# Kernel tuning notes

Hardware: AMD Instinct MI355X
Metric: run time of the kernel (lower is better)

## Reference

```python
import jax, jax.numpy as jnp
import numpy as np

N = 100000   # nodes
E = 1600000  # edges (avg degree 16)
F_IN = 128
HID = 128
C_OUT = 10
BN_EPS = 1e-5


def setup_inputs() -> dict:
    key = jax.random.key(0)
    ks = jax.random.split(key, 20)
    x = jax.random.normal(ks[0], (N, F_IN), jnp.float32)
    src = jax.random.randint(ks[1], (E,), 0, N)
    dst = jax.random.randint(ks[2], (E,), 0, N)
    def lin(k, fi, fo):
        return jax.random.normal(k, (fi, fo), jnp.float32) * (1.0 / np.sqrt(fi))
    inp = {
        "x": x, "src": src, "dst": dst,
        "W1": lin(ks[3], F_IN, HID), "b1": jnp.zeros((HID,), jnp.float32),
        "g1": jax.random.normal(ks[4], (HID,), jnp.float32) * 0.1 + 1.0,
        "be1": jax.random.normal(ks[5], (HID,), jnp.float32) * 0.1,
        "m1": jax.random.normal(ks[6], (HID,), jnp.float32) * 0.1,
        "v1": jax.random.uniform(ks[7], (HID,), jnp.float32, 0.5, 1.5),
        "W2": lin(ks[8], HID, HID), "b2": jnp.zeros((HID,), jnp.float32),
        "g2": jax.random.normal(ks[9], (HID,), jnp.float32) * 0.1 + 1.0,
        "be2": jax.random.normal(ks[10], (HID,), jnp.float32) * 0.1,
        "m2": jax.random.normal(ks[11], (HID,), jnp.float32) * 0.1,
        "v2": jax.random.uniform(ks[12], (HID,), jnp.float32, 0.5, 1.5),
        "W3": lin(ks[13], HID, C_OUT), "b3": jnp.zeros((C_OUT,), jnp.float32),
    }
    return inp


def _gcn_conv(x, W, b, src, dst):
    # PyG GCNConv: linear, add self-loops, symmetric deg^-1/2 normalization, scatter-add.
    h = x @ W                                            # [N, out]
    deg = jax.ops.segment_sum(jnp.ones((E,), h.dtype), dst, num_segments=N) + 1.0  # self-loop
    dinv = jax.lax.rsqrt(deg)                            # deg^{-1/2}, [N]
    coef = dinv[src] * dinv[dst]                         # per-edge norm, [E]
    agg = jax.ops.segment_sum(h[src] * coef[:, None], dst, num_segments=N)
    agg = agg + h * (dinv * dinv)[:, None]               # self-loop contribution
    return agg + b


def _bn_eval(x, g, be, m, v):
    return (x - m) * jax.lax.rsqrt(v + BN_EPS) * g + be


def reference(x, src, dst, W1, b1, g1, be1, m1, v1,
              W2, b2, g2, be2, m2, v2, W3, b3):
    h = jax.nn.relu(_bn_eval(_gcn_conv(x, W1, b1, src, dst), g1, be1, m1, v1))
    h = jax.nn.relu(_bn_eval(_gcn_conv(h, W2, b2, src, dst), g2, be2, m2, v2))
    return _gcn_conv(h, W3, b3, src, dst)                # [N, C_OUT] logits
```

## Files before the change

kernel.cpp:

```cpp
#include <hip/hip_runtime.h>

#define NN 100000
#define NE 1600000
#define FD 128
#define CO 10
#define BN_EPS 1e-5f
#define NBUK 782
#define NBUKP 784
#define BCAP 3072
#define SEGE 4096
#define NSEG 391

typedef __attribute__((ext_vector_type(8))) short short8;
typedef __attribute__((ext_vector_type(4))) float f32x4;

__device__ __forceinline__ unsigned short f2bf(float f) {
  unsigned int u = __builtin_bit_cast(unsigned int, f);
  u = (u + 0x7FFFu + ((u >> 16) & 1u)) >> 16;
  return (unsigned short)u;
}
__device__ __forceinline__ float bf2f(unsigned short h) {
  unsigned int u = ((unsigned int)h) << 16;
  return __builtin_bit_cast(float, u);
}
__device__ __forceinline__ float blo(unsigned int u) {
  return __builtin_bit_cast(float, u << 16);
}
__device__ __forceinline__ float bhi(unsigned int u) {
  return __builtin_bit_cast(float, u & 0xFFFF0000u);
}
__device__ __forceinline__ unsigned int cvt_pk_bf16(float a, float b) {
  unsigned int r;
  asm("v_cvt_pk_bf16_f32 %0, %1, %2" : "=v"(r) : "v"(a), "v"(b));
  return r;
}

__global__ __launch_bounds__(256) void k_hist_prep(
    const int* __restrict__ dst, int* __restrict__ histM,
    const float* __restrict__ W1, const float* __restrict__ W2,
    unsigned short* __restrict__ w1hi, unsigned short* __restrict__ w1lo,
    unsigned short* __restrict__ w2hi, unsigned short* __restrict__ w2lo,
    const float* __restrict__ b1, const float* __restrict__ g1,
    const float* __restrict__ be1, const float* __restrict__ m1,
    const float* __restrict__ v1,
    const float* __restrict__ b2, const float* __restrict__ g2,
    const float* __restrict__ be2, const float* __restrict__ m2,
    const float* __restrict__ v2,
    float* __restrict__ sc1, float* __restrict__ sh1,
    float* __restrict__ sc2, float* __restrict__ sh2) {
  __shared__ int hist[NBUK];
  int b = blockIdx.x, t = threadIdx.x;
  if (b < NSEG) {
    for (int i = t; i < NBUK; i += 256) hist[i] = 0;
    __syncthreads();
    int e0 = b * SEGE, e1 = min(e0 + SEGE, NE);
    for (int e = e0 + t; e < e1; e += 256) atomicAdd(&hist[dst[e] >> 7], 1);
    __syncthreads();
    for (int i = t; i < NBUK; i += 256) histM[b * NBUKP + i] = hist[i];
  } else if (b < NSEG + 128) {
    int bb = b - NSEG;
    const float* W = (bb < 64) ? W1 : W2;
    unsigned short* whi = (bb < 64) ? w1hi : w2hi;
    unsigned short* wlo = (bb < 64) ? w1lo : w2lo;
    int i = (bb & 63) * 256 + t;
    int k = i >> 7, n = i & 127;
    float w = W[i];
    unsigned short h = f2bf(w);
    unsigned short l = f2bf(w - bf2f(h));
    int idx = ((((k >> 5) * 8) + (n >> 4)) * 64 + ((k >> 3) & 3) * 16 + (n & 15)) * 8 + (k & 7);
    whi[idx] = h;
    wlo[idx] = l;
  } else {
    if (t < FD) {
      float s = g1[t] * rsqrtf(v1[t] + BN_EPS);
      sc1[t] = s;
      sh1[t] = (b1[t] - m1[t]) * s + be1[t];
    } else if (t < 2 * FD) {
      int f = t - FD;
      float s = g2[f] * rsqrtf(v2[f] + BN_EPS);
      sc2[f] = s;
      sh2[f] = (b2[f] - m2[f]) * s + be2[f];
    }
  }
}

__global__ __launch_bounds__(256) void k_colscan(const int* __restrict__ histM,
                                                 int* __restrict__ segbase,
                                                 int* __restrict__ btot) {
  __shared__ int lds[256];
  int b = blockIdx.x, t = threadIdx.x;
  int s0 = t * 2, s1 = t * 2 + 1;
  int v0 = (s0 < NSEG) ? histM[s0 * NBUKP + b] : 0;
  int v1 = (s1 < NSEG) ? histM[s1 * NBUKP + b] : 0;
  int pair = v0 + v1;
  lds[t] = pair;
  __syncthreads();
  int mine = pair;
  for (int off = 1; off < 256; off <<= 1) {
    int add = (t >= off) ? lds[t - off] : 0;
    __syncthreads();
    lds[t] += add;
    __syncthreads();
  }
  int run = lds[t] - mine;
  if (s0 < NSEG) segbase[s0 * NBUKP + b] = run;
  if (s1 < NSEG) segbase[s1 * NBUKP + b] = run + v0;
  if (t == 255) btot[b] = lds[255];
}

__global__ __launch_bounds__(256) void k_scatter2(const int* __restrict__ src,
                                                  const int* __restrict__ dst,
                                                  const int* __restrict__ segbase,
                                                  unsigned int* __restrict__ buck) {
  __shared__ int base[NBUK];
  int b = blockIdx.x, t = threadIdx.x;
  for (int i = t; i < NBUK; i += 256) base[i] = segbase[b * NBUKP + i];
  __syncthreads();
  int e0 = b * SEGE, e1 = min(e0 + SEGE, NE);
  for (int e = e0 + t; e < e1; e += 256) {
    int s = src[e], d = dst[e];
    int bk = d >> 7;
    int slot = atomicAdd(&base[bk], 1);
    buck[(size_t)bk * BCAP + slot] = ((unsigned int)(d & 127) << 17) | (unsigned int)s;
  }
}

__global__ __launch_bounds__(256) void k_finalize(const int* __restrict__ btot,
                                                  const unsigned int* __restrict__ buck,
                                                  uint4* __restrict__ nrange,
                                                  int* __restrict__ csr_src) {
  __shared__ unsigned int ebuf[BCAP];
  __shared__ int cnt[128];
  __shared__ int xoff[128];
  int b = blockIdx.x, t = threadIdx.x;
  int nb = btot[b];
  const unsigned int* bp = buck + (size_t)b * BCAP;
  for (int i = t; i < nb; i += 256) ebuf[i] = bp[i];
  if (t < 128) cnt[t] = 0;
  __syncthreads();
  for (int i = t; i < nb; i += 256) atomicAdd(&cnt[ebuf[i] >> 17], 1);
  __syncthreads();
  if (t < 128) xoff[t] = cnt[t];
  __syncthreads();
  for (int off = 1; off < 128; off <<= 1) {
    int add = 0;
    if (t < 128 && t >= off) add = xoff[t - off];
    __syncthreads();
    if (t < 128) xoff[t] += add;
    __syncthreads();
  }
  if (t < 128) {
    int node = b * 128 + t;
    int ex = xoff[t] - cnt[t];
    if (node < NN) {
      uint4 nr;
      nr.x = (unsigned)(b * BCAP + ex);
      nr.y = (unsigned)cnt[t];
      nr.z = __builtin_bit_cast(unsigned int, rsqrtf((float)cnt[t] + 1.0f));
      nr.w = 0;
      nrange[node] = nr;
    }
    xoff[t] = ex;
    cnt[t] = 0;
  }
  __syncthreads();
  int base = b * BCAP;
  for (int i = t; i < nb; i += 256) {
    unsigned int p = ebuf[i];
    int dl = (int)(p >> 17);
    int l = atomicAdd(&cnt[dl], 1);
    csr_src[base + xoff[dl] + l] = (int)(p & 0x1FFFFu);
  }
}

__global__ __launch_bounds__(256) void k_gemm128_mfma(const float* __restrict__ X,
                                                      const unsigned short* __restrict__ whi,
                                                      const unsigned short* __restrict__ wlo,
                                                      const uint4* __restrict__ nrange,
                                                      unsigned short* __restrict__ Hbs,
                                                      int nrows) {
  int tid = threadIdx.x;
  int lane = tid & 63, wv = tid >> 6;
  int lg = lane >> 4, li = lane & 15;
  int wr0 = blockIdx.x * 64 + wv * 16;
  int row = wr0 + li;
  bool ok = row < nrows;

  short8 ahi[4], alo[4];
#pragma unroll
  for (int ks = 0; ks < 4; ++ks) {
    if (ok) {
      const float* xp = X + (unsigned)(row * FD + ks * 32 + lg * 8);
      float4 v0 = *(const float4*)xp;
      float4 v1 = *(const float4*)(xp + 4);
      float f[8] = {v0.x, v0.y, v0.z, v0.w, v1.x, v1.y, v1.z, v1.w};
      unsigned int hp[4], lp[4];
#pragma unroll
      for (int j = 0; j < 4; ++j) {
        float a = f[2 * j], c = f[2 * j + 1];
        hp[j] = cvt_pk_bf16(a, c);
        float ra = a - blo(hp[j]);
        float rc = c - bhi(hp[j]);
        lp[j] = cvt_pk_bf16(ra, rc);
      }
      uint4 hv = {hp[0], hp[1], hp[2], hp[3]};
      uint4 lv = {lp[0], lp[1], lp[2], lp[3]};
      ahi[ks] = __builtin_bit_cast(short8, hv);
      alo[ks] = __builtin_bit_cast(short8, lv);
    } else {
#pragma unroll
      for (int j = 0; j < 8; ++j) { ahi[ks][j] = 0; alo[ks][j] = 0; }
    }
  }

  int rb = wr0 + lg * 4;
  float dvr[4];
#pragma unroll
  for (int r = 0; r < 4; ++r)
    dvr[r] = (rb + r < nrows) ? __builtin_bit_cast(float, nrange[rb + r].z) : 0.f;

#pragma unroll
  for (int nt = 0; nt < 8; ++nt) {
    f32x4 acc = {0.f, 0.f, 0.f, 0.f};
#pragma unroll
    for (int ks = 0; ks < 4; ++ks) {
      unsigned int bidx = (unsigned)(((ks * 8 + nt) * 64 + lane) * 8);
      short8 bh = *(const short8*)&whi[bidx];
      short8 bl = *(const short8*)&wlo[bidx];
      acc = __builtin_amdgcn_mfma_f32_16x16x32_bf16(ahi[ks], bh, acc, 0, 0, 0);
      acc = __builtin_amdgcn_mfma_f32_16x16x32_bf16(alo[ks], bh, acc, 0, 0, 0);
      acc = __builtin_amdgcn_mfma_f32_16x16x32_bf16(ahi[ks], bl, acc, 0, 0, 0);
    }
    int col = nt * 16 + li;
#pragma unroll
    for (int r = 0; r < 4; ++r) {
      if (rb + r < nrows)
        Hbs[(unsigned)((rb + r) * FD + col)] = f2bf(acc[r] * dvr[r]);
    }
  }
}

__global__ __launch_bounds__(256) void k_gather128(const uint4* __restrict__ nrange,
                                                   const int* __restrict__ csr_src,
                                                   const unsigned short* __restrict__ Hbs,
                                                   const float* __restrict__ sc,
                                                   const float* __restrict__ sh,
                                                   float* __restrict__ AGG) {
  int node = blockIdx.x * 4 + (threadIdx.x >> 6);
  node = __builtin_amdgcn_readfirstlane(node);
  int lane = threadIdx.x & 63;
  const unsigned int* Hc = (const unsigned int*)Hbs;
  uint4 nr = nrange[node];
  int beg = (int)nr.x, end = (int)(nr.x + nr.y);
  float dv = __builtin_bit_cast(float, nr.z);
  float px0, px1 = 0.f, px2 = 0.f, px3 = 0.f;
  float py0, py1 = 0.f, py2 = 0.f, py3 = 0.f;
  {
    unsigned int us = Hc[(unsigned)(node * 64) + lane];
    px0 = blo(us); py0 = bhi(us);
  }
  int e = beg;
  for (; e + 3 < end; e += 4) {
    unsigned int u0 = Hc[((unsigned)csr_src[e + 0] << 6) + lane];
    unsigned int u1 = Hc[((unsigned)csr_src[e + 1] << 6) + lane];
    unsigned int u2 = Hc[((unsigned)csr_src[e + 2] << 6) + lane];
    unsigned int u3 = Hc[((unsigned)csr_src[e + 3] << 6) + lane];
    px0 += blo(u0); py0 += bhi(u0);
    px1 += blo(u1); py1 += bhi(u1);
    px2 += blo(u2); py2 += bhi(u2);
    px3 += blo(u3); py3 += bhi(u3);
  }
  for (; e < end; ++e) {
    unsigned int u0 = Hc[((unsigned)csr_src[e] << 6) + lane];
    px0 += blo(u0); py0 += bhi(u0);
  }
  float accx = ((px0 + px1) + (px2 + px3)) * dv;
  float accy = ((py0 + py1) + (py2 + py3)) * dv;
  float scx = sc[lane * 2], scy = sc[lane * 2 + 1];
  float shx = sh[lane * 2], shy = sh[lane * 2 + 1];
  accx = fmaxf(fmaf(accx, scx, shx), 0.f);
  accy = fmaxf(fmaf(accy, scy, shy), 0.f);
  float2 o; o.x = accx; o.y = accy;
  ((float2*)AGG)[(unsigned)(node * 64) + lane] = o;
}

__global__ __launch_bounds__(256) void k_gather128_out(const uint4* __restrict__ nrange,
                                                       const int* __restrict__ csr_src,
                                                       const unsigned short* __restrict__ Hbs,
                                                       const float* __restrict__ sc,
                                                       const float* __restrict__ sh,
                                                       const float* __restrict__ W3,
                                                       float* __restrict__ H3s) {
  int node = blockIdx.x * 4 + (threadIdx.x >> 6);
  node = __builtin_amdgcn_readfirstlane(node);
  int lane = threadIdx.x & 63;
  float w3r[20];
  {
    const float* wp = W3 + lane * 2 * CO;
#pragma unroll
    for (int j = 0; j < 20; ++j) w3r[j] = wp[j];
  }
  const unsigned int* Hc = (const unsigned int*)Hbs;
  uint4 nr = nrange[node];
  int beg = (int)nr.x, end = (int)(nr.x + nr.y);
  float dv = __builtin_bit_cast(float, nr.z);
  float px0, px1 = 0.f, px2 = 0.f, px3 = 0.f;
  float py0, py1 = 0.f, py2 = 0.f, py3 = 0.f;
  {
    unsigned int us = Hc[(unsigned)(node * 64) + lane];
    px0 = blo(us); py0 = bhi(us);
  }
  int e = beg;
  for (; e + 3 < end; e += 4) {
    unsigned int u0 = Hc[((unsigned)csr_src[e + 0] << 6) + lane];
    unsigned int u1 = Hc[((unsigned)csr_src[e + 1] << 6) + lane];
    unsigned int u2 = Hc[((unsigned)csr_src[e + 2] << 6) + lane];
    unsigned int u3 = Hc[((unsigned)csr_src[e + 3] << 6) + lane];
    px0 += blo(u0); py0 += bhi(u0);
    px1 += blo(u1); py1 += bhi(u1);
    px2 += blo(u2); py2 += bhi(u2);
    px3 += blo(u3); py3 += bhi(u3);
  }
  for (; e < end; ++e) {
    unsigned int u0 = Hc[((unsigned)csr_src[e] << 6) + lane];
    px0 += blo(u0); py0 += bhi(u0);
  }
  float accx = ((px0 + px1) + (px2 + px3)) * dv;
  float accy = ((py0 + py1) + (py2 + py3)) * dv;
  float scx = sc[lane * 2], scy = sc[lane * 2 + 1];
  float shx = sh[lane * 2], shy = sh[lane * 2 + 1];
  accx = fmaxf(fmaf(accx, scx, shx), 0.f);
  accy = fmaxf(fmaf(accy, scy, shy), 0.f);
  float p[10];
#pragma unroll
  for (int c = 0; c < CO; ++c) p[c] = fmaf(accx, w3r[c], accy * w3r[10 + c]);
#pragma unroll
  for (int off = 32; off >= 1; off >>= 1) {
#pragma unroll
    for (int c = 0; c < CO; ++c) p[c] += __shfl_xor(p[c], off);
  }
#pragma unroll
  for (int c = 0; c < CO; ++c)
    if (lane == c) H3s[(unsigned)(node * CO + c)] = p[c] * dv;
}

__global__ __launch_bounds__(256) void k_gather10(const uint4* __restrict__ nrange,
                                                  const int* __restrict__ csr_src,
                                                  const float* __restrict__ H3s,
                                                  const float* __restrict__ b3,
                                                  float* __restrict__ out) {
  int node = blockIdx.x * 16 + (threadIdx.x >> 4);
  if (node >= NN) return;
  int c = threadIdx.x & 15;
  uint4 nr = nrange[node];
  int beg = (int)nr.x, end = (int)(nr.x + nr.y);
  float dv = __builtin_bit_cast(float, nr.z);
  float acc = 0.f;
  if (c < CO) acc = H3s[(unsigned)(node * CO + c)];
  for (int e = beg; e < end; ++e) {
    int s = csr_src[e];
    if (c < CO) acc += H3s[(unsigned)(s * CO + c)];
  }
  if (c < CO) out[(unsigned)(node * CO + c)] = fmaf(acc, dv, b3[c]);
}

extern "C" void kernel_launch(void* const* d_in, const int* in_sizes, int n_in,
                              void* d_out, int out_size, void* d_ws, size_t ws_size,
                              hipStream_t stream) {
  const float* x = (const float*)d_in[0];
  const int* src = (const int*)d_in[1];
  const int* dst = (const int*)d_in[2];
  const float* W1 = (const float*)d_in[3];
  const float* b1 = (const float*)d_in[4];
  const float* g1 = (const float*)d_in[5];
  const float* be1 = (const float*)d_in[6];
  const float* m1 = (const float*)d_in[7];
  const float* v1 = (const float*)d_in[8];
  const float* W2 = (const float*)d_in[9];
  const float* b2 = (const float*)d_in[10];
  const float* g2 = (const float*)d_in[11];
  const float* be2 = (const float*)d_in[12];
  const float* m2 = (const float*)d_in[13];
  const float* v2 = (const float*)d_in[14];
  const float* W3 = (const float*)d_in[15];
  const float* b3 = (const float*)d_in[16];
  float* out = (float*)d_out;

  char* wsb = (char*)d_ws;
  int* histM = (int*)wsb;                      wsb += (size_t)NSEG * NBUKP * 4;
  int* segbase = (int*)wsb;                    wsb += (size_t)NSEG * NBUKP * 4;
  int* btot = (int*)wsb;                       wsb += NBUKP * 4;
  uint4* nrange = (uint4*)wsb;                 wsb += (size_t)NN * 16;
  float* sc1 = (float*)wsb;                    wsb += FD * 4;
  float* sh1 = (float*)wsb;                    wsb += FD * 4;
  float* sc2 = (float*)wsb;                    wsb += FD * 4;
  float* sh2 = (float*)wsb;                    wsb += FD * 4;
  unsigned short* w1hi = (unsigned short*)wsb; wsb += FD * FD * 2;
  unsigned short* w1lo = (unsigned short*)wsb; wsb += FD * FD * 2;
  unsigned short* w2hi = (unsigned short*)wsb; wsb += FD * FD * 2;
  unsigned short* w2lo = (unsigned short*)wsb; wsb += FD * FD * 2;
  int* csr_src = (int*)wsb;                    wsb += (size_t)NBUK * BCAP * 4;
  unsigned int* buck = (unsigned int*)wsb;     wsb += (size_t)NBUK * BCAP * 4;
  float* AGG = (float*)wsb;                    wsb += (size_t)NN * FD * 4;
  unsigned short* Hbs = (unsigned short*)wsb;  wsb += (size_t)NN * FD * 2;
  float* H3s = (float*)wsb;                    wsb += (size_t)NN * CO * 4;

  k_hist_prep<<<NSEG + 129, 256, 0, stream>>>(dst, histM, W1, W2,
                                              w1hi, w1lo, w2hi, w2lo,
                                              b1, g1, be1, m1, v1,
                                              b2, g2, be2, m2, v2,
                                              sc1, sh1, sc2, sh2);
  k_colscan<<<NBUK, 256, 0, stream>>>(histM, segbase, btot);
  k_scatter2<<<NSEG, 256, 0, stream>>>(src, dst, segbase, buck);
  k_finalize<<<NBUK, 256, 0, stream>>>(btot, buck, nrange, csr_src);

  int gemm_blocks = (NN + 63) / 64;
  int gat_blocks = (NN + 3) / 4;

  k_gemm128_mfma<<<gemm_blocks, 256, 0, stream>>>(x, w1hi, w1lo, nrange, Hbs, NN);
  k_gather128<<<gat_blocks, 256, 0, stream>>>(nrange, csr_src, Hbs, sc1, sh1, AGG);
  k_gemm128_mfma<<<gemm_blocks, 256, 0, stream>>>(AGG, w2hi, w2lo, nrange, Hbs, NN);
  k_gather128_out<<<gat_blocks, 256, 0, stream>>>(nrange, csr_src, Hbs, sc2, sh2, W3, H3s);
  k_gather10<<<(NN + 15) / 16, 256, 0, stream>>>(nrange, csr_src, H3s, b3, out);
}
```

Before: 313.9 us.

## Store layer-1 activations as bf16, add bf16-A GEMM, pad H3, double edge segments

The first gather now writes its normalized, ReLU'd activations as packed bf16 instead of fp32. A new GEMM kernel loads these bf16 rows directly and drops the lo-part A MFMA, which cuts activation memory traffic and MFMA count for layer 2. Separately, the layer-3 intermediate is padded to 16 floats per node for aligned gathers, and the edge segment size doubles, halving the number of histogram/scatter blocks so the column scan handles one segment per thread. These choices lose precision in the layer-2 input, and the scatter kernel ends up with fewer, longer-running blocks.

```diff
diff --git a/kernel.cpp b/kernel.cpp
--- a/kernel.cpp
+++ b/kernel.cpp
@@ -8,8 +8,9 @@
 #define NBUK 782
 #define NBUKP 784
 #define BCAP 3072
-#define SEGE 4096
-#define NSEG 391
+#define SEGE 8192
+#define NSEG 196
+#define H3P 16
 
 typedef __attribute__((ext_vector_type(8))) short short8;
 typedef __attribute__((ext_vector_type(4))) float f32x4;
@@ -89,22 +90,17 @@
                                                  int* __restrict__ btot) {
   __shared__ int lds[256];
   int b = blockIdx.x, t = threadIdx.x;
-  int s0 = t * 2, s1 = t * 2 + 1;
-  int v0 = (s0 < NSEG) ? histM[s0 * NBUKP + b] : 0;
-  int v1 = (s1 < NSEG) ? histM[s1 * NBUKP + b] : 0;
-  int pair = v0 + v1;
-  lds[t] = pair;
-  __syncthreads();
-  int mine = pair;
+  int v = (t < NSEG) ? histM[t * NBUKP + b] : 0;
+  lds[t] = v;
+  __syncthreads();
+  int mine = v;
   for (int off = 1; off < 256; off <<= 1) {
     int add = (t >= off) ? lds[t - off] : 0;
     __syncthreads();
     lds[t] += add;
     __syncthreads();
   }
-  int run = lds[t] - mine;
-  if (s0 < NSEG) segbase[s0 * NBUKP + b] = run;
-  if (s1 < NSEG) segbase[s1 * NBUKP + b] = run + v0;
+  if (t < NSEG) segbase[t * NBUKP + b] = lds[t] - mine;
   if (t == 255) btot[b] = lds[255];
 }
 
@@ -240,12 +236,62 @@
   }
 }
 
+__global__ __launch_bounds__(256) void k_gemm128_bf16A(const unsigned short* __restrict__ Ab,
+                                                       const unsigned short* __restrict__ whi,
+                                                       const unsigned short* __restrict__ wlo,
+                                                       const uint4* __restrict__ nrange,
+                                                       unsigned short* __restrict__ Hbs,
+                                                       int nrows) {
+  int tid = threadIdx.x;
+  int lane = tid & 63, wv = tid >> 6;
+  int lg = lane >> 4, li = lane & 15;
+  int wr0 = blockIdx.x * 64 + wv * 16;
+  int row = wr0 + li;
+  bool ok = row < nrows;
+
+  short8 ahi[4];
+#pragma unroll
+  for (int ks = 0; ks < 4; ++ks) {
+    if (ok) {
+      ahi[ks] = *(const short8*)(Ab + (unsigned)(row * FD + ks * 32 + lg * 8));
+    } else {
+#pragma unroll
+      for (int j = 0; j < 8; ++j) ahi[ks][j] = 0;
+    }
+  }
+
+  int rb = wr0 + lg * 4;
+  float dvr[4];
+#pragma unroll
+  for (int r = 0; r < 4; ++r)
+    dvr[r] = (rb + r < nrows) ? __builtin_bit_cast(float, nrange[rb + r].z) : 0.f;
+
+#pragma unroll
+  for (int nt = 0; nt < 8; ++nt) {
+    f32x4 acc = {0.f, 0.f, 0.f, 0.f};
+#pragma unroll
+    for (int ks = 0; ks < 4; ++ks) {
+      unsigned int bidx = (unsigned)(((ks * 8 + nt) * 64 + lane) * 8);
+      short8 bh = *(const short8*)&whi[bidx];
+      short8 bl = *(const short8*)&wlo[bidx];
+      acc = __builtin_amdgcn_mfma_f32_16x16x32_bf16(ahi[ks], bh, acc, 0, 0, 0);
+      acc = __builtin_amdgcn_mfma_f32_16x16x32_bf16(ahi[ks], bl, acc, 0, 0, 0);
+    }
+    int col = nt * 16 + li;
+#pragma unroll
+    for (int r = 0; r < 4; ++r) {
+      if (rb + r < nrows)
+        Hbs[(unsigned)((rb + r) * FD + col)] = f2bf(acc[r] * dvr[r]);
+    }
+  }
+}
+
 __global__ __launch_bounds__(256) void k_gather128(const uint4* __restrict__ nrange,
                                                    const int* __restrict__ csr_src,
                                                    const unsigned short* __restrict__ Hbs,
                                                    const float* __restrict__ sc,
                                                    const float* __restrict__ sh,
-                                                   float* __restrict__ AGG) {
+                                                   unsigned int* __restrict__ AGGb) {
   int node = blockIdx.x * 4 + (threadIdx.x >> 6);
   node = __builtin_amdgcn_readfirstlane(node);
   int lane = threadIdx.x & 63;
@@ -280,8 +326,7 @@
   float shx = sh[lane * 2], shy = sh[lane * 2 + 1];
   accx = fmaxf(fmaf(accx, scx, shx), 0.f);
   accy = fmaxf(fmaf(accy, scy, shy), 0.f);
-  float2 o; o.x = accx; o.y = accy;
-  ((float2*)AGG)[(unsigned)(node * 64) + lane] = o;
+  AGGb[(unsigned)(node * 64) + lane] = cvt_pk_bf16(accx, accy);
 }
 
 __global__ __launch_bounds__(256) void k_gather128_out(const uint4* __restrict__ nrange,
@@ -341,7 +386,7 @@
   }
 #pragma unroll
   for (int c = 0; c < CO; ++c)
-    if (lane == c) H3s[(unsigned)(node * CO + c)] = p[c] * dv;
+    if (lane == c) H3s[(unsigned)(node * H3P + c)] = p[c] * dv;
 }
 
 __global__ __launch_bounds__(256) void k_gather10(const uint4* __restrict__ nrange,
@@ -356,10 +401,10 @@
   int beg = (int)nr.x, end = (int)(nr.x + nr.y);
   float dv = __builtin_bit_cast(float, nr.z);
   float acc = 0.f;
-  if (c < CO) acc = H3s[(unsigned)(node * CO + c)];
+  if (c < CO) acc = H3s[(unsigned)(node * H3P + c)];
   for (int e = beg; e < end; ++e) {
     int s = csr_src[e];
-    if (c < CO) acc += H3s[(unsigned)(s * CO + c)];
+    if (c < CO) acc += H3s[(unsigned)(s * H3P + c)];
   }
   if (c < CO) out[(unsigned)(node * CO + c)] = fmaf(acc, dv, b3[c]);
 }
@@ -401,9 +446,9 @@
   unsigned short* w2lo = (unsigned short*)wsb; wsb += FD * FD * 2;
   int* csr_src = (int*)wsb;                    wsb += (size_t)NBUK * BCAP * 4;
   unsigned int* buck = (unsigned int*)wsb;     wsb += (size_t)NBUK * BCAP * 4;
-  float* AGG = (float*)wsb;                    wsb += (size_t)NN * FD * 4;
+  unsigned int* AGGb = (unsigned int*)wsb;     wsb += (size_t)NN * FD * 2;
   unsigned short* Hbs = (unsigned short*)wsb;  wsb += (size_t)NN * FD * 2;
-  float* H3s = (float*)wsb;                    wsb += (size_t)NN * CO * 4;
+  float* H3s = (float*)wsb;                    wsb += (size_t)NN * H3P * 4;
 
   k_hist_prep<<<NSEG + 129, 256, 0, stream>>>(dst, histM, W1, W2,
                                               w1hi, w1lo, w2hi, w2lo,
@@ -418,8 +463,9 @@
   int gat_blocks = (NN + 3) / 4;
 
   k_gemm128_mfma<<<gemm_blocks, 256, 0, stream>>>(x, w1hi, w1lo, nrange, Hbs, NN);
-  k_gather128<<<gat_blocks, 256, 0, stream>>>(nrange, csr_src, Hbs, sc1, sh1, AGG);
-  k_gemm128_mfma<<<gemm_blocks, 256, 0, stream>>>(AGG, w2hi, w2lo, nrange, Hbs, NN);
+  k_gather128<<<gat_blocks, 256, 0, stream>>>(nrange, csr_src, Hbs, sc1, sh1, AGGb);
+  k_gemm128_bf16A<<<gemm_blocks, 256, 0, stream>>>((const unsigned short*)AGGb,
+                                                   w2hi, w2lo, nrange, Hbs, NN);
   k_gather128_out<<<gat_blocks, 256, 0, stream>>>(nrange, csr_src, Hbs, sc2, sh2, W3, H3s);
   k_gather10<<<(NN + 15) / 16, 256, 0, stream>>>(nrange, csr_src, H3s, b3, out);
 }
```

Result: no change. 310.7 us (-1.0%).
